# Performance work log

Hardware: AMD Instinct MI355X
Metric: run time of the kernel (lower is better)

## Reference

```python
import jax, jax.numpy as jnp
import numpy as np
from jax import lax

B, D, N = 1024, 1024, 65536
M, Ks, DS = 8, 256, 128      # key PQ: subvectors, codewords, subvec dim (D/M)
MV, DV = 8, 256              # value PQ: subvectors, subvec dim (OUT/MV)
OUT = MV * DV
K_TOP = 64


def setup_inputs() -> dict:
    key = jax.random.key(0)
    ks = jax.random.split(key, 7)
    x = jax.random.normal(ks[0], (B, D), dtype=jnp.float32)
    # whitening matrix starts as identity in the module; perturb slightly for a non-trivial test
    whitening_matrix = jnp.eye(D, dtype=jnp.float32) + 0.01 * jax.random.normal(ks[1], (D, D), dtype=jnp.float32)
    key_codebooks = jax.random.normal(ks[2], (M, Ks, DS), dtype=jnp.float32)
    value_codebooks = jax.random.normal(ks[3], (MV, Ks, DV), dtype=jnp.float32)
    bias = jnp.zeros((OUT,), dtype=jnp.float32)
    key_codes = jax.random.randint(ks[4], (N, M), 0, Ks, dtype=jnp.int32)
    value_codes = jax.random.randint(ks[5], (N, MV), 0, Ks, dtype=jnp.int32)
    return {
        "x": x,
        "whitening_matrix": whitening_matrix,
        "key_codebooks": key_codebooks,
        "value_codebooks": value_codebooks,
        "bias": bias,
        "key_codes": key_codes,
        "value_codes": value_codes,
        "k": K_TOP,
    }


def reference(x, whitening_matrix, key_codebooks, value_codebooks, bias, key_codes, value_codes, k):
    # 1) whiten the query (module buffer 'whitening_matrix')
    q = x @ whitening_matrix                      # [B, D]
    qs = q.reshape(B, M, DS)                      # [B, M, DS] query subvectors

    # 2) ADC distance tables: squared L2 between each query subvector and each codeword
    #    dt[b, m, c] = ||qs[b,m] - cb[m,c]||^2
    q_sq = jnp.sum(qs * qs, axis=-1)              # [B, M]
    c_sq = jnp.sum(key_codebooks * key_codebooks, axis=-1)  # [M, Ks]
    cross = jnp.einsum("bmd,mcd->bmc", qs, key_codebooks)   # [B, M, Ks]
    dt = q_sq[:, :, None] + c_sq[None, :, :] - 2.0 * cross  # [B, M, Ks]

    # 3) asymmetric distance to all N stored keys via code gather (irregular access)
    lut = dt.transpose(1, 0, 2)                   # [M, B, Ks]
    # per-subvector gather then sum: d[b, n] = sum_m lut[m, b, key_codes[n, m]]
    dists = jax.vmap(lambda l, c: l[:, c])(lut, key_codes.T).sum(axis=0)  # [B, N]

    # 4) top-k nearest neighbors
    neg_top, top_idx = lax.top_k(-dists, k)       # [B, k]

    # 5) reconstruct values of retrieved neighbors from value PQ codebooks
    vc = value_codes[top_idx]                     # [B, k, MV] int codes
    vals = value_codebooks[jnp.arange(MV)[None, None, :], vc]  # [B, k, MV, DV]
    vals = vals.reshape(vals.shape[0], vals.shape[1], OUT)      # [B, k, OUT]

    # 6) distance-weighted aggregation (softmax over negative distances) + bias
    w = jax.nn.softmax(neg_top, axis=-1)          # [B, k]
    y = jnp.einsum("bk,bko->bo", w, vals) + bias  # [B, OUT]
    return y
```

## Files before the change

kernel.cpp:

```cpp
#include <hip/hip_runtime.h>

#define N_ITEMS 65536

__launch_bounds__(256)
__global__ void gemm_q_kernel(const float* __restrict__ A,
                              const float* __restrict__ W,
                              float* __restrict__ qpart) {
  __shared__ float As[16][132];
  __shared__ float Bs[16][132];
  const int tid = threadIdx.x;
  const int tx = tid & 15, ty = tid >> 4;
  const int rb = blockIdx.y * 128, cb = blockIdx.x * 128;
  const int kz = blockIdx.z * 128;
  const int ar = tid >> 2, ac = (tid & 3) << 2;
  const int bk = tid >> 5, bc = (tid & 31) << 2;

  float4 va0 = *(const float4*)&A[(rb + ar) * 1024 + kz + ac];
  float4 va1 = *(const float4*)&A[(rb + ar + 64) * 1024 + kz + ac];
  float4 vb0 = *(const float4*)&W[(kz + bk) * 1024 + cb + bc];
  float4 vb1 = *(const float4*)&W[(kz + bk + 8) * 1024 + cb + bc];

  float acc[8][8] = {};
  for (int k0 = 0; k0 < 128; k0 += 16) {
    As[ac + 0][ar] = va0.x; As[ac + 1][ar] = va0.y;
    As[ac + 2][ar] = va0.z; As[ac + 3][ar] = va0.w;
    As[ac + 0][ar + 64] = va1.x; As[ac + 1][ar + 64] = va1.y;
    As[ac + 2][ar + 64] = va1.z; As[ac + 3][ar + 64] = va1.w;
    *(float4*)&Bs[bk][bc] = vb0;
    *(float4*)&Bs[bk + 8][bc] = vb1;
    __syncthreads();
    if (k0 + 16 < 128) {
      va0 = *(const float4*)&A[(rb + ar) * 1024 + kz + k0 + 16 + ac];
      va1 = *(const float4*)&A[(rb + ar + 64) * 1024 + kz + k0 + 16 + ac];
      vb0 = *(const float4*)&W[(kz + k0 + 16 + bk) * 1024 + cb + bc];
      vb1 = *(const float4*)&W[(kz + k0 + 16 + bk + 8) * 1024 + cb + bc];
    }
#pragma unroll
    for (int kk = 0; kk < 16; kk++) {
      const float4 a0 = *(const float4*)&As[kk][ty << 2];
      const float4 a1 = *(const float4*)&As[kk][64 + (ty << 2)];
      const float4 b0 = *(const float4*)&Bs[kk][tx << 2];
      const float4 b1 = *(const float4*)&Bs[kk][64 + (tx << 2)];
      const float ar8[8] = {a0.x, a0.y, a0.z, a0.w, a1.x, a1.y, a1.z, a1.w};
      const float br8[8] = {b0.x, b0.y, b0.z, b0.w, b1.x, b1.y, b1.z, b1.w};
#pragma unroll
      for (int r = 0; r < 8; r++)
#pragma unroll
        for (int c = 0; c < 8; c++)
          acc[r][c] = fmaf(ar8[r], br8[c], acc[r][c]);
    }
    __syncthreads();
  }
  float* outp = qpart + blockIdx.z * 1048576;
#pragma unroll
  for (int rh = 0; rh < 2; rh++)
#pragma unroll
    for (int r = 0; r < 4; r++) {
      const int row = rb + rh * 64 + (ty << 2) + r;
      const int ri = rh * 4 + r;
      *(float4*)&outp[row * 1024 + cb + (tx << 2)] =
          make_float4(acc[ri][0], acc[ri][1], acc[ri][2], acc[ri][3]);
      *(float4*)&outp[row * 1024 + cb + 64 + (tx << 2)] =
          make_float4(acc[ri][4], acc[ri][5], acc[ri][6], acc[ri][7]);
    }
}

__launch_bounds__(256)
__global__ void qsum_kernel(const float4* __restrict__ qp,
                            float4* __restrict__ q) {
  const int i = blockIdx.x * 256 + threadIdx.x;
  float4 s0 = qp[i];
  float4 s1 = qp[i + 131072];
#pragma unroll
  for (int z = 1; z < 8; z++) {
    const float4 a = qp[z * 262144 + i];
    const float4 b = qp[z * 262144 + i + 131072];
    s0.x += a.x; s0.y += a.y; s0.z += a.z; s0.w += a.w;
    s1.x += b.x; s1.y += b.y; s1.z += b.z; s1.w += b.w;
  }
  q[i] = s0;
  q[i + 131072] = s1;
}

__launch_bounds__(256)
__global__ void lut_kernel(const float* __restrict__ q,
                           const float* __restrict__ kcb,
                           const int* __restrict__ key_codes,
                           float* __restrict__ lut,
                           unsigned long long* __restrict__ pcodes,
                           uint4* __restrict__ poffs) {
  if (blockIdx.z == 8) {
    const int g0 = (((int)blockIdx.y * 4 + (int)blockIdx.x) * 256 + (int)threadIdx.x) * 4;
#pragma unroll
    for (int t = 0; t < 4; t++) {
      const int gid = g0 + t;
      unsigned long long p = 0ull;
      unsigned h[8];
#pragma unroll
      for (int j = 0; j < 8; j++) {
        const unsigned c = (unsigned)key_codes[gid * 8 + j] & 255u;
        p |= (unsigned long long)c << (8 * j);
        h[j] = c * 36u;
      }
      pcodes[gid] = p;
      poffs[gid] = make_uint4(h[0] | (h[1] << 16), h[2] | (h[3] << 16),
                              h[4] | (h[5] << 16), h[6] | (h[7] << 16));
    }
    return;
  }

  __shared__ float As[32][68];
  __shared__ float Bs[32][68];
  const int tid = threadIdx.x;
  const int tx = tid & 15, ty = tid >> 4;
  const int m = blockIdx.z;
  const int rb = blockIdx.y * 64;
  const int cb0 = blockIdx.x * 64;
  float acc[4][4] = {};
  float qa[4] = {}, cs[4] = {};
  for (int k0 = 0; k0 < 128; k0 += 32) {
#pragma unroll
    for (int l = 0; l < 2; l++) {
      const int e = tid + l * 256;
      const int row = e >> 3, c4 = (e & 7) << 2;
      const float4 va = *(const float4*)&q[(rb + row) * 1024 + m * 128 + k0 + c4];
      As[c4 + 0][row] = va.x; As[c4 + 1][row] = va.y;
      As[c4 + 2][row] = va.z; As[c4 + 3][row] = va.w;
      const float4 vb = *(const float4*)&kcb[(m * 256 + cb0 + row) * 128 + k0 + c4];
      Bs[c4 + 0][row] = vb.x; Bs[c4 + 1][row] = vb.y;
      Bs[c4 + 2][row] = vb.z; Bs[c4 + 3][row] = vb.w;
    }
    __syncthreads();
#pragma unroll
    for (int kk = 0; kk < 32; kk++) {
      const float4 a = *(const float4*)&As[kk][ty << 2];
      const float4 b = *(const float4*)&Bs[kk][tx << 2];
      const float ar[4] = {a.x, a.y, a.z, a.w};
      const float br[4] = {b.x, b.y, b.z, b.w};
#pragma unroll
      for (int r = 0; r < 4; r++)
#pragma unroll
        for (int c = 0; c < 4; c++)
          acc[r][c] = fmaf(ar[r], br[c], acc[r][c]);
#pragma unroll
      for (int r = 0; r < 4; r++) qa[r] = fmaf(ar[r], ar[r], qa[r]);
#pragma unroll
      for (int c = 0; c < 4; c++) cs[c] = fmaf(br[c], br[c], cs[c]);
    }
    __syncthreads();
  }
#pragma unroll
  for (int r = 0; r < 4; r++) {
    const int row = rb + (ty << 2) + r;
    const int col = cb0 + (tx << 2);
    float4 v;
    v.x = qa[r] + cs[0] - 2.0f * acc[r][0];
    v.y = qa[r] + cs[1] - 2.0f * acc[r][1];
    v.z = qa[r] + cs[2] - 2.0f * acc[r][2];
    v.w = qa[r] + cs[3] - 2.0f * acc[r][3];
    *(float4*)&lut[row * 2048 + m * 256 + col] = v;
  }
}

extern __shared__ char dyn_lds[];

__launch_bounds__(1024)
__global__ void scansel_kernel(const float* __restrict__ lutf,
                               const uint4* __restrict__ poffs,
                               const unsigned long long* __restrict__ pcodes,
                               const int* __restrict__ value_codes,
                               const float* __restrict__ vcb,
                               float* __restrict__ partials,
                               float2* __restrict__ mW) {
  char* repb = dyn_lds;
  unsigned char* temps = (unsigned char*)(dyn_lds + 73728);
  unsigned* tempw = (unsigned*)(dyn_lds + 73728);
  const int tid = threadIdx.x;
  const int g = blockIdx.x >> 1;
  const int hf = blockIdx.x & 1;

  {
    const int w = tid >> 6, lane = tid & 63;
#pragma unroll
    for (int t0 = 0; t0 < 2; t0++) {
      const int t = w + t0 * 16;
      const int rr = t & 3, seg = t >> 2;
      const int row = (g << 2) + rr;
      const int e0 = seg * 256 + lane * 4;
      const float4 v4 = *(const float4*)&lutf[row * 2048 + e0];
      float s4 = v4.x + v4.y + v4.z + v4.w;
#pragma unroll
      for (int off = 32; off > 0; off >>= 1) s4 += __shfl_xor(s4, off);
      const float mean = s4 * (1.0f / 256.0f);
      const float vals[4] = {v4.x, v4.y, v4.z, v4.w};
#pragma unroll
      for (int k = 0; k < 4; k++) {
        int iv = (int)rintf(vals[k] - mean);
        iv = max(-127, min(127, iv));
        temps[(e0 + k) * 4 + rr] = (unsigned char)(iv + 128);
      }
    }
  }
  __syncthreads();

  {
    const unsigned v0 = tempw[tid * 2];
    const unsigned v1 = tempw[tid * 2 + 1];
    unsigned* repw = (unsigned*)dyn_lds;
    const int d0 = tid * 18;
#pragma unroll
    for (int r2 = 0; r2 < 8; r2++) {
      repw[d0 + r2] = v0;
      repw[d0 + 9 + r2] = v1;
    }
  }
  __syncthreads();

  const int r = tid & 7;
  const char* base0 = repb + (r << 2);
  const char* base1 = repb + 36864 + (r << 2);
  unsigned k0[4], k1[4];
#pragma unroll
  for (int j = 0; j < 4; j++) { k0[j] = 0xFFFFFFFFu; k1[j] = 0xFFFFFFFFu; }

  unsigned A[8], B[8];

  auto issue = [&](unsigned (&BUF)[8], const uint4 cw) {
    BUF[0] = *(const unsigned*)(base0 + (cw.x & 0xFFFFu));
    BUF[1] = *(const unsigned*)(base0 + (cw.x >> 16) + 9216);
    BUF[2] = *(const unsigned*)(base0 + (cw.y & 0xFFFFu) + 18432);
    BUF[3] = *(const unsigned*)(base0 + (cw.y >> 16) + 27648);
    BUF[4] = *(const unsigned*)(base1 + (cw.z & 0xFFFFu));
    BUF[5] = *(const unsigned*)(base1 + (cw.z >> 16) + 9216);
    BUF[6] = *(const unsigned*)(base1 + (cw.w & 0xFFFFu) + 18432);
    BUF[7] = *(const unsigned*)(base1 + (cw.w >> 16) + 27648);
  };

  auto consume = [&](const unsigned (&BUF)[8], const int it) {
    const unsigned M = 0x00FF00FFu;
    unsigned accA = BUF[0] & M;
    unsigned accB = (BUF[0] >> 8) & M;
#pragma unroll
    for (int j = 1; j < 8; j++) {
      accA += BUF[j] & M;
      accB += (BUF[j] >> 8) & M;
    }
    const int ss[4] = {(int)(accA & 0xFFFFu), (int)(accB & 0xFFFFu),
                       (int)(accA >> 16), (int)(accB >> 16)};
#pragma unroll
    for (int j = 0; j < 4; j++) {
      const unsigned key = ((unsigned)ss[j] << 6) | (unsigned)it;
      const unsigned mx = (k0[j] > key) ? k0[j] : key;
      k0[j] = (k0[j] < key) ? k0[j] : key;
      k1[j] = (k1[j] < mx) ? k1[j] : mx;
    }
  };

  const int nb = (hf << 15) + tid;
  {
    const uint4 cA = poffs[nb];
    issue(A, cA);
  }
  uint4 cNxt = poffs[nb + 1024];

  for (int it = 0; it < 32; it += 2) {
    const uint4 c2 = poffs[nb + (((it + 2) & 31) << 10)];
    const uint4 c3 = poffs[nb + (((it + 3) & 31) << 10)];
    issue(B, cNxt);
    consume(A, it);
    issue(A, c2);
    consume(B, it + 1);
    cNxt = c3;
  }

  __syncthreads();

  unsigned* cl  = (unsigned*)dyn_lds;
  float* wts    = (float*)(dyn_lds + 4096);
  unsigned long long* sv8 = (unsigned long long*)(dyn_lds + 8192);
  float* gred   = (float*)(dyn_lds + 16384);
  unsigned* rmin = (unsigned*)(dyn_lds + 16448);
  int* rcnt     = (int*)(dyn_lds + 16464);
  float* dmin4  = (float*)(dyn_lds + 16480);
  float* wsum4  = (float*)(dyn_lds + 16496);

  if (tid < 4) { rmin[tid] = 0xFFFFFFFFu; rcnt[tid] = 0; }
  __syncthreads();

#pragma unroll
  for (int j = 0; j < 4; j++) {
    unsigned d = k0[j] >> 6;
#pragma unroll
    for (int off = 32; off > 0; off >>= 1) {
      const unsigned o = __shfl_xor(d, off);
      d = (o < d) ? o : d;
    }
    if ((tid & 63) == 0) atomicMin(&rmin[j], d);
  }
  __syncthreads();

  {
    const int lane = tid & 63;
    const unsigned long long lm = (1ull << lane) - 1ull;
#pragma unroll
    for (int j = 0; j < 4; j++) {
      const unsigned lim = rmin[j] + 20u;
#pragma unroll
      for (int c = 0; c < 2; c++) {
        const unsigned key = c ? k1[j] : k0[j];
        const unsigned d = key >> 6;
        const bool pred = d <= lim;
        const unsigned long long m = __ballot(pred);
        int base = 0;
        if (lane == 0 && m) base = atomicAdd(&rcnt[j], __popcll(m));
        base = __shfl(base, 0);
        if (pred) {
          const int pos = base + __popcll(m & lm);
          if (pos < 256)
            cl[j * 256 + pos] = (d << 16) | ((key & 63u) << 10) | (unsigned)tid;
        }
      }
    }
  }
  __syncthreads();

  const int gj = tid >> 8, gt = tid & 255;
  const int cnt_g = min(rcnt[gj], 256);
  float dex = 1e30f;
  if (gt < cnt_g) {
    const unsigned pc = cl[gj * 256 + gt];
    const int n = (hf << 15) + (int)(pc & 0xFFFFu);
    const unsigned long long c8 = pcodes[n];
    const uint4 vc0 = *(const uint4*)&value_codes[n * 8];
    const uint4 vc1 = *(const uint4*)&value_codes[n * 8 + 4];
    sv8[gj * 256 + gt] =
        (unsigned long long)(vc0.x & 255u)        | ((unsigned long long)(vc0.y & 255u) << 8)  |
        ((unsigned long long)(vc0.z & 255u) << 16) | ((unsigned long long)(vc0.w & 255u) << 24) |
        ((unsigned long long)(vc1.x & 255u) << 32) | ((unsigned long long)(vc1.y & 255u) << 40) |
        ((unsigned long long)(vc1.z & 255u) << 48) | ((unsigned long long)(vc1.w & 255u) << 56);
    const float* lrow = lutf + ((g << 2) + gj) * 2048;
    const unsigned lo = (unsigned)c8, hi = (unsigned)(c8 >> 32);
    dex  = lrow[        (lo       & 255u)];
    dex += lrow[ 256 + ((lo >>  8) & 255u)];
    dex += lrow[ 512 + ((lo >> 16) & 255u)];
    dex += lrow[ 768 + ((lo >> 24)       )];
    dex += lrow[1024 + ( hi        & 255u)];
    dex += lrow[1280 + ((hi >>  8) & 255u)];
    dex += lrow[1536 + ((hi >> 16) & 255u)];
    dex += lrow[1792 + ((hi >> 24)       )];
  }
  float mnf = dex;
#pragma unroll
  for (int off = 32; off > 0; off >>= 1) mnf = fminf(mnf, __shfl_xor(mnf, off));
  if ((tid & 63) == 0) gred[gj * 4 + ((tid >> 6) & 3)] = mnf;
  __syncthreads();
  const float dminx = fminf(fminf(gred[gj * 4], gred[gj * 4 + 1]),
                            fminf(gred[gj * 4 + 2], gred[gj * 4 + 3]));
  const float w = (gt < cnt_g) ? __expf(dminx - dex) : 0.f;
  wts[gj * 256 + gt] = w;
  float sw_ = w;
#pragma unroll
  for (int off = 32; off > 0; off >>= 1) sw_ += __shfl_xor(sw_, off);
  __syncthreads();
  if ((tid & 63) == 0) gred[gj * 4 + ((tid >> 6) & 3)] = sw_;
  __syncthreads();
  if (gt == 0) {
    dmin4[gj] = dminx;
    wsum4[gj] = gred[gj * 4] + gred[gj * 4 + 1] + gred[gj * 4 + 2] + gred[gj * 4 + 3];
  }
  __syncthreads();

  if (tid < 4)
    mW[((g << 2) + tid) * 2 + hf] = make_float2(dmin4[tid], wsum4[tid]);

  const int hp = tid >> 9, u = tid & 511;
  const int col = u << 2;
  const int mv = col >> 8;
  const int co = col & 255;
  const float* vb2 = vcb + mv * 65536 + co;
#pragma unroll
  for (int jr = 0; jr < 2; jr++) {
    const int j = (jr << 1) | hp;
    const int row = (g << 2) + j;
    const int cj = min(rcnt[j], 256);
    float4 acc = make_float4(0.f, 0.f, 0.f, 0.f);
    int k = 0;
    for (; k + 1 < cj; k += 2) {
      const float w0 = wts[j * 256 + k];
      const float w1 = wts[j * 256 + k + 1];
      const unsigned c0 = (unsigned)((sv8[j * 256 + k] >> (mv * 8)) & 255ull);
      const unsigned c1 = (unsigned)((sv8[j * 256 + k + 1] >> (mv * 8)) & 255ull);
      const float4 v0 = *(const float4*)(vb2 + c0 * 256);
      const float4 v1 = *(const float4*)(vb2 + c1 * 256);
      acc.x = fmaf(w0, v0.x, acc.x); acc.y = fmaf(w0, v0.y, acc.y);
      acc.z = fmaf(w0, v0.z, acc.z); acc.w = fmaf(w0, v0.w, acc.w);
      acc.x = fmaf(w1, v1.x, acc.x); acc.y = fmaf(w1, v1.y, acc.y);
      acc.z = fmaf(w1, v1.z, acc.z); acc.w = fmaf(w1, v1.w, acc.w);
    }
    if (k < cj) {
      const float w0 = wts[j * 256 + k];
      const unsigned c0 = (unsigned)((sv8[j * 256 + k] >> (mv * 8)) & 255ull);
      const float4 v0 = *(const float4*)(vb2 + c0 * 256);
      acc.x = fmaf(w0, v0.x, acc.x); acc.y = fmaf(w0, v0.y, acc.y);
      acc.z = fmaf(w0, v0.z, acc.z); acc.w = fmaf(w0, v0.w, acc.w);
    }
    *(float4*)&partials[((row << 1) + hf) * 2048 + col] = acc;
  }
}

__launch_bounds__(256)
__global__ void combine_kernel(const float* __restrict__ partials,
                               const float2* __restrict__ mW,
                               const float* __restrict__ bias,
                               float* __restrict__ out) {
  const int row = blockIdx.x;
  const int t = threadIdx.x;
  const float2 mw0 = mW[row * 2];
  const float2 mw1 = mW[row * 2 + 1];
  const float m = fminf(mw0.x, mw1.x);
  const float a0 = __expf(m - mw0.x);
  const float a1 = __expf(m - mw1.x);
  const float inv = 1.0f / fmaf(a0, mw0.y, a1 * mw1.y);
  const int c = t * 8;
  const float* p0 = partials + (row * 2) * 2048 + c;
  const float* p1 = partials + (row * 2 + 1) * 2048 + c;
#pragma unroll
  for (int v = 0; v < 2; v++) {
    const float4 x0 = *(const float4*)(p0 + v * 4);
    const float4 x1 = *(const float4*)(p1 + v * 4);
    const float4 bb = *(const float4*)&bias[c + v * 4];
    float4 o;
    o.x = fmaf(fmaf(a0, x0.x, a1 * x1.x), inv, bb.x);
    o.y = fmaf(fmaf(a0, x0.y, a1 * x1.y), inv, bb.y);
    o.z = fmaf(fmaf(a0, x0.z, a1 * x1.z), inv, bb.z);
    o.w = fmaf(fmaf(a0, x0.w, a1 * x1.w), inv, bb.w);
    *(float4*)&out[row * 2048 + c + v * 4] = o;
  }
}

__launch_bounds__(512)
__global__ void scan16_kernel(const float* __restrict__ lut,
                              const unsigned long long* __restrict__ pcodes,
                              unsigned* __restrict__ cand_d,
                              unsigned short* __restrict__ cand_n) {
  __shared__ short sRep[32768];
  const int tid = threadIdx.x;
  const int b = blockIdx.x;

  const float4 v4 = *(const float4*)&lut[b * 2048 + tid * 4];
  float s4 = v4.x + v4.y + v4.z + v4.w;
#pragma unroll
  for (int off = 32; off > 0; off >>= 1) s4 += __shfl_xor(s4, off);
  const float mean = s4 * (1.0f / 256.0f);

  const float vals[4] = {v4.x, v4.y, v4.z, v4.w};
#pragma unroll
  for (int k2 = 0; k2 < 4; k2++) {
    float f = (vals[k2] - mean) * 64.0f;
    f = fmaxf(fminf(f, 32000.0f), -32000.0f);
    const int iv = (int)rintf(f);
    const unsigned hw = (unsigned)(unsigned short)iv;
    const unsigned wrd = hw | (hw << 16);
    const uint4 wv = make_uint4(wrd, wrd, wrd, wrd);
    const int e = tid * 4 + k2;
    *(uint4*)&((unsigned*)sRep)[e * 8] = wv;
    *(uint4*)&((unsigned*)sRep)[e * 8 + 4] = wv;
  }
  __syncthreads();

  const int r = tid & 15;
  int d0 = 0x7FFFFFFF, d1 = 0x7FFFFFFF, d2 = 0x7FFFFFFF, d3 = 0x7FFFFFFF;
  int i0 = 0, i1 = 0, i2 = 0, i3 = 0;

  unsigned long long c8 = pcodes[tid];
  for (int it = 0; it < 128; it++) {
    const int n = tid + (it << 9);
    unsigned long long nxt = 0ull;
    if (it < 127) nxt = pcodes[n + 512];
    const unsigned lo = (unsigned)c8;
    const unsigned hi = (unsigned)(c8 >> 32);
    int s;
    s  = sRep[(((lo      ) & 255u) << 4) + r        ];
    s += sRep[(((lo >>  8) & 255u) << 4) + r +  4096];
    s += sRep[(((lo >> 16) & 255u) << 4) + r +  8192];
    s += sRep[(((lo >> 24)       ) << 4) + r + 12288];
    s += sRep[(((hi      ) & 255u) << 4) + r + 16384];
    s += sRep[(((hi >>  8) & 255u) << 4) + r + 20480];
    s += sRep[(((hi >> 16) & 255u) << 4) + r + 24576];
    s += sRep[(((hi >> 24)       ) << 4) + r + 28672];
    if (s < d3) {
      if (s < d1) {
        if (s < d0) { d3 = d2; i3 = i2; d2 = d1; i2 = i1; d1 = d0; i1 = i0; d0 = s; i0 = n; }
        else        { d3 = d2; i3 = i2; d2 = d1; i2 = i1; d1 = s; i1 = n; }
      } else {
        if (s < d2) { d3 = d2; i3 = i2; d2 = s; i2 = n; }
        else        { d3 = s; i3 = n; }
      }
    }
    c8 = nxt;
  }

  const int base = b * 2048 + tid * 4;
  const uint4 dv = make_uint4((unsigned)(d0 + 0x40000000), (unsigned)(d1 + 0x40000000),
                              (unsigned)(d2 + 0x40000000), (unsigned)(d3 + 0x40000000));
  *(uint4*)&cand_d[base] = dv;
  const unsigned ni01 = (unsigned)i0 | ((unsigned)i1 << 16);
  const unsigned ni23 = (unsigned)i2 | ((unsigned)i3 << 16);
  *(uint2*)&cand_n[base] = make_uint2(ni01, ni23);
}

__launch_bounds__(256)
__global__ void select_kernel(const unsigned* __restrict__ cand_d,
                              const unsigned short* __restrict__ cand_n,
                              const int* __restrict__ value_codes,
                              const float* __restrict__ vcb,
                              const float* __restrict__ bias,
                              const unsigned long long* __restrict__ pcodes,
                              const float* __restrict__ lutf,
                              const unsigned lim_add,
                              float* __restrict__ out) {
  __shared__ unsigned sredw[4];
  __shared__ float sredf[4];
  __shared__ unsigned long long clist[256];
  __shared__ float sw[256];
  __shared__ int svc[2048];
  __shared__ int scnt;
  __shared__ float sWsum;

  const int tid = threadIdx.x;
  const int b = blockIdx.x;

  const uint4 a0 = *(const uint4*)&cand_d[b * 2048 + tid * 8];
  const uint4 a1 = *(const uint4*)&cand_d[b * 2048 + tid * 8 + 4];
  const uint4 nn = *(const uint4*)&cand_n[b * 2048 + tid * 8];
  unsigned dk[8] = {a0.x, a0.y, a0.z, a0.w, a1.x, a1.y, a1.z, a1.w};
  unsigned ni[8] = {nn.x & 0xFFFFu, nn.x >> 16, nn.y & 0xFFFFu, nn.y >> 16,
                    nn.z & 0xFFFFu, nn.z >> 16, nn.w & 0xFFFFu, nn.w >> 16};

  if (tid == 0) scnt = 0;
  unsigned mn = dk[0];
#pragma unroll
  for (int j = 1; j < 8; j++) mn = (dk[j] < mn) ? dk[j] : mn;
#pragma unroll
  for (int off = 32; off > 0; off >>= 1) {
    const unsigned o = __shfl_xor(mn, off);
    mn = (o < mn) ? o : mn;
  }
  if ((tid & 63) == 0) sredw[tid >> 6] = mn;
  __syncthreads();
  unsigned sMin = sredw[0];
  sMin = (sredw[1] < sMin) ? sredw[1] : sMin;
  sMin = (sredw[2] < sMin) ? sredw[2] : sMin;
  sMin = (sredw[3] < sMin) ? sredw[3] : sMin;
  const unsigned lim = sMin + lim_add;

  const int lane = tid & 63;
  const unsigned long long lm = (1ull << lane) - 1ull;
#pragma unroll
  for (int j = 0; j < 8; j++) {
    const bool pred = dk[j] <= lim;
    const unsigned long long mask = __ballot(pred);
    int base = 0;
    if (lane == 0 && mask) base = atomicAdd(&scnt, __popcll(mask));
    base = __shfl(base, 0);
    if (pred) {
      const int pos = base + __popcll(mask & lm);
      if (pos < 256) clist[pos] = ((unsigned long long)dk[j] << 32) | ni[j];
    }
  }
  __syncthreads();
  const int cnt = min(scnt, 256);

  float dex = 1e30f;
  if (tid < cnt) {
    const int n = (int)(clist[tid] & 0xFFFFFFFFu);
    const unsigned long long c8 = pcodes[n];
    const float* lrow = lutf + b * 2048;
    const unsigned lo = (unsigned)c8, hi = (unsigned)(c8 >> 32);
    dex  = lrow[        (lo       & 255u)];
    dex += lrow[ 256 + ((lo >>  8) & 255u)];
    dex += lrow[ 512 + ((lo >> 16) & 255u)];
    dex += lrow[ 768 + ((lo >> 24)       )];
    dex += lrow[1024 + ( hi        & 255u)];
    dex += lrow[1280 + ((hi >>  8) & 255u)];
    dex += lrow[1536 + ((hi >> 16) & 255u)];
    dex += lrow[1792 + ((hi >> 24)       )];
  }
  for (int i = tid; i < (cnt << 3); i += 256)
    svc[i] = value_codes[((int)(clist[i >> 3] & 0xFFFFFFFFu)) * 8 + (i & 7)];
  float mnf = dex;
#pragma unroll
  for (int off = 32; off > 0; off >>= 1) mnf = fminf(mnf, __shfl_xor(mnf, off));
  if ((tid & 63) == 0) sredf[tid >> 6] = mnf;
  __syncthreads();
  const float dminx = fminf(fminf(sredf[0], sredf[1]), fminf(sredf[2], sredf[3]));
  if (tid < cnt) sw[tid] = __expf(dminx - dex);
  __syncthreads();

  if (tid < 64) {
    float s = 0.f;
    for (int j = tid; j < cnt; j += 64) s += sw[j];
#pragma unroll
    for (int off = 32; off > 0; off >>= 1) s += __shfl_xor(s, off);
    if (tid == 0) sWsum = s;
  }
  __syncthreads();
  const float inv = 1.0f / sWsum;

  const int c0 = tid << 3;
  const int mv = c0 >> 8;
  const int off = c0 & 255;
  float4 acc0 = make_float4(0.f, 0.f, 0.f, 0.f);
  float4 acc1 = make_float4(0.f, 0.f, 0.f, 0.f);
  const float* vbase = vcb + mv * 65536 + off;
  for (int k = 0; k < cnt; k++) {
    const float w = sw[k];
    const float* vp = vbase + svc[(k << 3) + mv] * 256;
    const float4 v0 = *(const float4*)vp;
    const float4 v1 = *(const float4*)(vp + 4);
    acc0.x = fmaf(w, v0.x, acc0.x); acc0.y = fmaf(w, v0.y, acc0.y);
    acc0.z = fmaf(w, v0.z, acc0.z); acc0.w = fmaf(w, v0.w, acc0.w);
    acc1.x = fmaf(w, v1.x, acc1.x); acc1.y = fmaf(w, v1.y, acc1.y);
    acc1.z = fmaf(w, v1.z, acc1.z); acc1.w = fmaf(w, v1.w, acc1.w);
  }
  const float4 b0 = *(const float4*)&bias[c0];
  const float4 b1 = *(const float4*)&bias[c0 + 4];
  *(float4*)&out[b * 2048 + c0] =
      make_float4(fmaf(acc0.x, inv, b0.x), fmaf(acc0.y, inv, b0.y),
                  fmaf(acc0.z, inv, b0.z), fmaf(acc0.w, inv, b0.w));
  *(float4*)&out[b * 2048 + c0 + 4] =
      make_float4(fmaf(acc1.x, inv, b1.x), fmaf(acc1.y, inv, b1.y),
                  fmaf(acc1.z, inv, b1.z), fmaf(acc1.w, inv, b1.w));
}

extern "C" void kernel_launch(void* const* d_in, const int* in_sizes, int n_in,
                              void* d_out, int out_size, void* d_ws, size_t ws_size,
                              hipStream_t stream) {
  const float* x    = (const float*)d_in[0];
  const float* W    = (const float*)d_in[1];
  const float* kcb  = (const float*)d_in[2];
  const float* vcb  = (const float*)d_in[3];
  const float* bias = (const float*)d_in[4];
  const int* key_codes   = (const int*)d_in[5];
  const int* value_codes = (const int*)d_in[6];
  float* out = (float*)d_out;

  float* qpart = (float*)d_ws;
  float* q     = qpart + 8388608;
  float* lut   = q + 1048576;
  uint4* poffs = (uint4*)(lut + 2097152);
  unsigned long long* pcodes = (unsigned long long*)(poffs + 65536);
  float* partials = (float*)(pcodes + 65536);
  float2* mW = (float2*)(partials + 4194304);
  unsigned* cand_d = (unsigned*)d_ws;
  unsigned short* cand_n = (unsigned short*)(cand_d + 2097152);

  hipLaunchKernelGGL(gemm_q_kernel, dim3(8, 8, 8), dim3(256), 0, stream,
                     x, W, qpart);
  hipLaunchKernelGGL(qsum_kernel, dim3(512), dim3(256), 0, stream,
                     (const float4*)qpart, (float4*)q);
  hipLaunchKernelGGL(lut_kernel, dim3(4, 16, 9), dim3(256), 0, stream,
                     q, kcb, key_codes, lut, pcodes, poffs);

  const hipError_t attr_rc = hipFuncSetAttribute(
      (const void*)scansel_kernel, hipFuncAttributeMaxDynamicSharedMemorySize, 81920);
  if (attr_rc == hipSuccess) {
    hipLaunchKernelGGL(scansel_kernel, dim3(512), dim3(1024), 81920, stream,
                       lut, poffs, pcodes, value_codes, vcb, partials, mW);
    hipLaunchKernelGGL(combine_kernel, dim3(1024), dim3(256), 0, stream,
                       partials, mW, bias, out);
  } else {
    hipLaunchKernelGGL(scan16_kernel, dim3(1024), dim3(512), 0, stream,
                       lut, pcodes, cand_d, cand_n);
    hipLaunchKernelGGL(select_kernel, dim3(1024), dim3(256), 0, stream,
                       cand_d, cand_n, value_codes, vcb, bias, pcodes, lut,
                       1024u, out);
  }
}
```

Before: 172.0 us.

## Process eight query rows per scan block using 64-bit LDS LUT gathers

The scan/select kernel now handles 8 query rows per block instead of 4. The quantized LUT bytes for 8 rows are interleaved so each code lookup gathers a uint2 covering all 8 rows, which halves the number of blocks and the code-offset loads per row. The intent is to amortize the poffs reads and LDS gather instructions over twice as many queries. The cost is a much larger dynamic LDS footprint (144 KB, which relies on MI355X's larger LDS) and more registers for the running top-2 keys, which lowers occupancy to one 1024-thread block per CU, with 256 blocks in the grid.

Result: slower. 177.7 us (+3.4%).

```diff
diff --git a/kernel.cpp b/kernel.cpp
--- a/kernel.cpp
+++ b/kernel.cpp
@@ -100,7 +100,7 @@
       for (int j = 0; j < 8; j++) {
         const unsigned c = (unsigned)key_codes[gid * 8 + j] & 255u;
         p |= (unsigned long long)c << (8 * j);
-        h[j] = c * 36u;
+        h[j] = c << 6;
       }
       pcodes[gid] = p;
       poffs[gid] = make_uint4(h[0] | (h[1] << 16), h[2] | (h[3] << 16),
@@ -173,8 +173,8 @@
                                float* __restrict__ partials,
                                float2* __restrict__ mW) {
   char* repb = dyn_lds;
-  unsigned char* temps = (unsigned char*)(dyn_lds + 73728);
-  unsigned* tempw = (unsigned*)(dyn_lds + 73728);
+  unsigned char* temps = (unsigned char*)(dyn_lds + 131072);
+  unsigned long long* tempq = (unsigned long long*)(dyn_lds + 131072);
   const int tid = threadIdx.x;
   const int g = blockIdx.x >> 1;
   const int hf = blockIdx.x & 1;
@@ -182,10 +182,10 @@
   {
     const int w = tid >> 6, lane = tid & 63;
 #pragma unroll
-    for (int t0 = 0; t0 < 2; t0++) {
+    for (int t0 = 0; t0 < 4; t0++) {
       const int t = w + t0 * 16;
-      const int rr = t & 3, seg = t >> 2;
-      const int row = (g << 2) + rr;
+      const int rr = t & 7, seg = t >> 3;
+      const int row = (g << 3) + rr;
       const int e0 = seg * 256 + lane * 4;
       const float4 v4 = *(const float4*)&lutf[row * 2048 + e0];
       float s4 = v4.x + v4.y + v4.z + v4.w;
@@ -197,58 +197,65 @@
       for (int k = 0; k < 4; k++) {
         int iv = (int)rintf(vals[k] - mean);
         iv = max(-127, min(127, iv));
-        temps[(e0 + k) * 4 + rr] = (unsigned char)(iv + 128);
+        temps[(e0 + k) * 8 + rr] = (unsigned char)(iv + 128);
       }
     }
   }
   __syncthreads();
 
   {
-    const unsigned v0 = tempw[tid * 2];
-    const unsigned v1 = tempw[tid * 2 + 1];
-    unsigned* repw = (unsigned*)dyn_lds;
-    const int d0 = tid * 18;
-#pragma unroll
-    for (int r2 = 0; r2 < 8; r2++) {
-      repw[d0 + r2] = v0;
-      repw[d0 + 9 + r2] = v1;
+    const int lane = tid & 63;
+    const unsigned long long q0 = tempq[tid * 2];
+    const unsigned long long q1 = tempq[tid * 2 + 1];
+    const uint4 w0 = make_uint4((unsigned)q0, (unsigned)(q0 >> 32),
+                                (unsigned)q0, (unsigned)(q0 >> 32));
+    const uint4 w1 = make_uint4((unsigned)q1, (unsigned)(q1 >> 32),
+                                (unsigned)q1, (unsigned)(q1 >> 32));
+    uint4* repv = (uint4*)dyn_lds;
+#pragma unroll
+    for (int k = 0; k < 4; k++) {
+      const int kk = (k + lane) & 3;
+      repv[tid * 8 + kk] = w0;
+      repv[tid * 8 + 4 + kk] = w1;
     }
   }
   __syncthreads();
 
   const int r = tid & 7;
-  const char* base0 = repb + (r << 2);
-  const char* base1 = repb + 36864 + (r << 2);
-  unsigned k0[4], k1[4];
-#pragma unroll
-  for (int j = 0; j < 4; j++) { k0[j] = 0xFFFFFFFFu; k1[j] = 0xFFFFFFFFu; }
-
-  unsigned A[8], B[8];
-
-  auto issue = [&](unsigned (&BUF)[8], const uint4 cw) {
-    BUF[0] = *(const unsigned*)(base0 + (cw.x & 0xFFFFu));
-    BUF[1] = *(const unsigned*)(base0 + (cw.x >> 16) + 9216);
-    BUF[2] = *(const unsigned*)(base0 + (cw.y & 0xFFFFu) + 18432);
-    BUF[3] = *(const unsigned*)(base0 + (cw.y >> 16) + 27648);
-    BUF[4] = *(const unsigned*)(base1 + (cw.z & 0xFFFFu));
-    BUF[5] = *(const unsigned*)(base1 + (cw.z >> 16) + 9216);
-    BUF[6] = *(const unsigned*)(base1 + (cw.w & 0xFFFFu) + 18432);
-    BUF[7] = *(const unsigned*)(base1 + (cw.w >> 16) + 27648);
+  const char* base0 = repb + (r << 3);
+  const char* base1 = repb + 65536 + (r << 3);
+  unsigned k0[8], k1[8];
+#pragma unroll
+  for (int j = 0; j < 8; j++) { k0[j] = 0xFFFFFFFFu; k1[j] = 0xFFFFFFFFu; }
+
+  uint2 A[8], B[8];
+
+  auto issue = [&](uint2 (&BUF)[8], const uint4 cw) {
+    BUF[0] = *(const uint2*)(base0 + (cw.x & 0xFFFFu));
+    BUF[1] = *(const uint2*)(base0 + (cw.x >> 16) + 16384);
+    BUF[2] = *(const uint2*)(base0 + (cw.y & 0xFFFFu) + 32768);
+    BUF[3] = *(const uint2*)(base0 + (cw.y >> 16) + 49152);
+    BUF[4] = *(const uint2*)(base1 + (cw.z & 0xFFFFu));
+    BUF[5] = *(const uint2*)(base1 + (cw.z >> 16) + 16384);
+    BUF[6] = *(const uint2*)(base1 + (cw.w & 0xFFFFu) + 32768);
+    BUF[7] = *(const uint2*)(base1 + (cw.w >> 16) + 49152);
   };
 
-  auto consume = [&](const unsigned (&BUF)[8], const int it) {
+  auto consume = [&](const uint2 (&BUF)[8], const int it) {
     const unsigned M = 0x00FF00FFu;
-    unsigned accA = BUF[0] & M;
-    unsigned accB = (BUF[0] >> 8) & M;
+    unsigned aA = BUF[0].x & M, aB = (BUF[0].x >> 8) & M;
+    unsigned aC = BUF[0].y & M, aD = (BUF[0].y >> 8) & M;
 #pragma unroll
     for (int j = 1; j < 8; j++) {
-      accA += BUF[j] & M;
-      accB += (BUF[j] >> 8) & M;
-    }
-    const int ss[4] = {(int)(accA & 0xFFFFu), (int)(accB & 0xFFFFu),
-                       (int)(accA >> 16), (int)(accB >> 16)};
-#pragma unroll
-    for (int j = 0; j < 4; j++) {
+      aA += BUF[j].x & M; aB += (BUF[j].x >> 8) & M;
+      aC += BUF[j].y & M; aD += (BUF[j].y >> 8) & M;
+    }
+    const int ss[8] = {(int)(aA & 0xFFFFu), (int)(aB & 0xFFFFu),
+                       (int)(aA >> 16),     (int)(aB >> 16),
+                       (int)(aC & 0xFFFFu), (int)(aD & 0xFFFFu),
+                       (int)(aC >> 16),     (int)(aD >> 16)};
+#pragma unroll
+    for (int j = 0; j < 8; j++) {
       const unsigned key = ((unsigned)ss[j] << 6) | (unsigned)it;
       const unsigned mx = (k0[j] > key) ? k0[j] : key;
       k0[j] = (k0[j] < key) ? k0[j] : key;
@@ -276,19 +283,19 @@
   __syncthreads();
 
   unsigned* cl  = (unsigned*)dyn_lds;
-  float* wts    = (float*)(dyn_lds + 4096);
-  unsigned long long* sv8 = (unsigned long long*)(dyn_lds + 8192);
-  float* gred   = (float*)(dyn_lds + 16384);
-  unsigned* rmin = (unsigned*)(dyn_lds + 16448);
-  int* rcnt     = (int*)(dyn_lds + 16464);
-  float* dmin4  = (float*)(dyn_lds + 16480);
-  float* wsum4  = (float*)(dyn_lds + 16496);
-
-  if (tid < 4) { rmin[tid] = 0xFFFFFFFFu; rcnt[tid] = 0; }
-  __syncthreads();
-
-#pragma unroll
-  for (int j = 0; j < 4; j++) {
+  float* wts    = (float*)(dyn_lds + 8192);
+  unsigned long long* sv8 = (unsigned long long*)(dyn_lds + 16384);
+  float* gred   = (float*)(dyn_lds + 32768);
+  unsigned* rmin = (unsigned*)(dyn_lds + 32832);
+  int* rcnt     = (int*)(dyn_lds + 32864);
+  float* dmin8  = (float*)(dyn_lds + 32896);
+  float* wsum8  = (float*)(dyn_lds + 32928);
+
+  if (tid < 8) { rmin[tid] = 0xFFFFFFFFu; rcnt[tid] = 0; }
+  __syncthreads();
+
+#pragma unroll
+  for (int j = 0; j < 8; j++) {
     unsigned d = k0[j] >> 6;
 #pragma unroll
     for (int off = 32; off > 0; off >>= 1) {
@@ -303,7 +310,7 @@
     const int lane = tid & 63;
     const unsigned long long lm = (1ull << lane) - 1ull;
 #pragma unroll
-    for (int j = 0; j < 4; j++) {
+    for (int j = 0; j < 8; j++) {
       const unsigned lim = rmin[j] + 20u;
 #pragma unroll
       for (int c = 0; c < 2; c++) {
@@ -324,54 +331,64 @@
   }
   __syncthreads();
 
-  const int gj = tid >> 8, gt = tid & 255;
+  const int gj = tid >> 7, gt = tid & 127;
   const int cnt_g = min(rcnt[gj], 256);
-  float dex = 1e30f;
-  if (gt < cnt_g) {
-    const unsigned pc = cl[gj * 256 + gt];
-    const int n = (hf << 15) + (int)(pc & 0xFFFFu);
-    const unsigned long long c8 = pcodes[n];
-    const uint4 vc0 = *(const uint4*)&value_codes[n * 8];
-    const uint4 vc1 = *(const uint4*)&value_codes[n * 8 + 4];
-    sv8[gj * 256 + gt] =
-        (unsigned long long)(vc0.x & 255u)        | ((unsigned long long)(vc0.y & 255u) << 8)  |
-        ((unsigned long long)(vc0.z & 255u) << 16) | ((unsigned long long)(vc0.w & 255u) << 24) |
-        ((unsigned long long)(vc1.x & 255u) << 32) | ((unsigned long long)(vc1.y & 255u) << 40) |
-        ((unsigned long long)(vc1.z & 255u) << 48) | ((unsigned long long)(vc1.w & 255u) << 56);
-    const float* lrow = lutf + ((g << 2) + gj) * 2048;
-    const unsigned lo = (unsigned)c8, hi = (unsigned)(c8 >> 32);
-    dex  = lrow[        (lo       & 255u)];
-    dex += lrow[ 256 + ((lo >>  8) & 255u)];
-    dex += lrow[ 512 + ((lo >> 16) & 255u)];
-    dex += lrow[ 768 + ((lo >> 24)       )];
-    dex += lrow[1024 + ( hi        & 255u)];
-    dex += lrow[1280 + ((hi >>  8) & 255u)];
-    dex += lrow[1536 + ((hi >> 16) & 255u)];
-    dex += lrow[1792 + ((hi >> 24)       )];
-  }
-  float mnf = dex;
+  float dex[2] = {1e30f, 1e30f};
+#pragma unroll
+  for (int s2 = 0; s2 < 2; s2++) {
+    const int ci = gt + (s2 << 7);
+    if (ci < cnt_g) {
+      const unsigned pc = cl[gj * 256 + ci];
+      const int n = (hf << 15) + (int)(pc & 0x7FFFu);
+      const unsigned long long c8 = pcodes[n];
+      const uint4 vc0 = *(const uint4*)&value_codes[n * 8];
+      const uint4 vc1 = *(const uint4*)&value_codes[n * 8 + 4];
+      sv8[gj * 256 + ci] =
+          (unsigned long long)(vc0.x & 255u)        | ((unsigned long long)(vc0.y & 255u) << 8)  |
+          ((unsigned long long)(vc0.z & 255u) << 16) | ((unsigned long long)(vc0.w & 255u) << 24) |
+          ((unsigned long long)(vc1.x & 255u) << 32) | ((unsigned long long)(vc1.y & 255u) << 40) |
+          ((unsigned long long)(vc1.z & 255u) << 48) | ((unsigned long long)(vc1.w & 255u) << 56);
+      const float* lrow = lutf + ((g << 3) + gj) * 2048;
+      const unsigned lo = (unsigned)c8, hi = (unsigned)(c8 >> 32);
+      float dx;
+      dx  = lrow[        (lo       & 255u)];
+      dx += lrow[ 256 + ((lo >>  8) & 255u)];
+      dx += lrow[ 512 + ((lo >> 16) & 255u)];
+      dx += lrow[ 768 + ((lo >> 24)       )];
+      dx += lrow[1024 + ( hi        & 255u)];
+      dx += lrow[1280 + ((hi >>  8) & 255u)];
+      dx += lrow[1536 + ((hi >> 16) & 255u)];
+      dx += lrow[1792 + ((hi >> 24)       )];
+      dex[s2] = dx;
+    }
+  }
+  float mnf = fminf(dex[0], dex[1]);
 #pragma unroll
   for (int off = 32; off > 0; off >>= 1) mnf = fminf(mnf, __shfl_xor(mnf, off));
-  if ((tid & 63) == 0) gred[gj * 4 + ((tid >> 6) & 3)] = mnf;
-  __syncthreads();
-  const float dminx = fminf(fminf(gred[gj * 4], gred[gj * 4 + 1]),
-                            fminf(gred[gj * 4 + 2], gred[gj * 4 + 3]));
-  const float w = (gt < cnt_g) ? __expf(dminx - dex) : 0.f;
-  wts[gj * 256 + gt] = w;
-  float sw_ = w;
-#pragma unroll
-  for (int off = 32; off > 0; off >>= 1) sw_ += __shfl_xor(sw_, off);
-  __syncthreads();
-  if ((tid & 63) == 0) gred[gj * 4 + ((tid >> 6) & 3)] = sw_;
+  if ((tid & 63) == 0) gred[gj * 2 + ((tid >> 6) & 1)] = mnf;
+  __syncthreads();
+  const float dminx = fminf(gred[gj * 2], gred[gj * 2 + 1]);
+  float wloc = 0.f;
+#pragma unroll
+  for (int s2 = 0; s2 < 2; s2++) {
+    const int ci = gt + (s2 << 7);
+    const float wv = (ci < cnt_g) ? __expf(dminx - dex[s2]) : 0.f;
+    wts[gj * 256 + ci] = wv;
+    wloc += wv;
+  }
+#pragma unroll
+  for (int off = 32; off > 0; off >>= 1) wloc += __shfl_xor(wloc, off);
+  __syncthreads();
+  if ((tid & 63) == 0) gred[gj * 2 + ((tid >> 6) & 1)] = wloc;
   __syncthreads();
   if (gt == 0) {
-    dmin4[gj] = dminx;
-    wsum4[gj] = gred[gj * 4] + gred[gj * 4 + 1] + gred[gj * 4 + 2] + gred[gj * 4 + 3];
-  }
-  __syncthreads();
-
-  if (tid < 4)
-    mW[((g << 2) + tid) * 2 + hf] = make_float2(dmin4[tid], wsum4[tid]);
+    dmin8[gj] = dminx;
+    wsum8[gj] = gred[gj * 2] + gred[gj * 2 + 1];
+  }
+  __syncthreads();
+
+  if (tid < 8)
+    mW[((g << 3) + tid) * 2 + hf] = make_float2(dmin8[tid], wsum8[tid]);
 
   const int hp = tid >> 9, u = tid & 511;
   const int col = u << 2;
@@ -379,9 +396,9 @@
   const int co = col & 255;
   const float* vb2 = vcb + mv * 65536 + co;
 #pragma unroll
-  for (int jr = 0; jr < 2; jr++) {
+  for (int jr = 0; jr < 4; jr++) {
     const int j = (jr << 1) | hp;
-    const int row = (g << 2) + j;
+    const int row = (g << 3) + j;
     const int cj = min(rcnt[j], 256);
     float4 acc = make_float4(0.f, 0.f, 0.f, 0.f);
     int k = 0;
@@ -663,9 +680,9 @@
                      q, kcb, key_codes, lut, pcodes, poffs);
 
   const hipError_t attr_rc = hipFuncSetAttribute(
-      (const void*)scansel_kernel, hipFuncAttributeMaxDynamicSharedMemorySize, 81920);
+      (const void*)scansel_kernel, hipFuncAttributeMaxDynamicSharedMemorySize, 147456);
   if (attr_rc == hipSuccess) {
-    hipLaunchKernelGGL(scansel_kernel, dim3(512), dim3(1024), 81920, stream,
+    hipLaunchKernelGGL(scansel_kernel, dim3(256), dim3(1024), 147456, stream,
                        lut, poffs, pcodes, value_codes, vcb, partials, mW);
     hipLaunchKernelGGL(combine_kernel, dim3(1024), dim3(256), 0, stream,
                        partials, mW, bias, out);
```
